# Kernel optimization log

Hardware: AMD Instinct MI355X
Metric: run time of the kernel (lower is better)

The kernel has to match this reference:

```python
import jax, jax.numpy as jnp
import numpy as np

DIM = 64  # per-head feature dim used for the 1/sqrt(dim) scale


def setup_inputs() -> dict:
    key = jax.random.key(0)
    kq, kk, kv, kw, kb = jax.random.split(key, 5)
    B, S, D, DK = 32, 4096, 64, 256
    q = jax.random.normal(kq, (B, S, D), dtype=jnp.float32)
    k = jax.random.normal(kk, (B, S, D), dtype=jnp.float32)
    v = jax.random.normal(kv, (B, S, D), dtype=jnp.float32)
    # Linear(input_size=S -> dim_k=DK): weight [DK, S], bias [DK]
    E_w = jax.random.normal(kw, (DK, S), dtype=jnp.float32) * (1.0 / np.sqrt(S))
    E_b = jax.random.normal(kb, (DK,), dtype=jnp.float32) * 0.01
    return {"q": q, "k": k, "v": v, "E_w": E_w, "E_b": E_b}


def reference(q, k, v, E_w, E_b):
    # K projection: k.transpose(1,2) -> [b, d, s]; E(k) -> [b, d, dim_k]
    K = jnp.einsum('bsd,ks->bdk', k, E_w) + E_b  # [b, d, dim_k]
    # scores = q @ K / sqrt(dim) -> [b, s, dim_k]
    scores = jnp.matmul(q, K) / jnp.sqrt(jnp.asarray(DIM, q.dtype))
    P_bar = jax.nn.softmax(scores, axis=-1)  # softmax over projected dim_k axis
    # V projection with F = E (parameter sharing): v -> [b, d, dim_k] -> transpose -> [b, dim_k, d]
    V = jnp.einsum('bsd,ks->bkd', v, E_w) + E_b[None, :, None]  # [b, dim_k, d]
    out = jnp.matmul(P_bar, V)  # [b, s, d]
    return out
```

## Files before the change

### kernel.cpp

```cpp
#include <hip/hip_runtime.h>
#include <hip/hip_bf16.h>
#include <stdint.h>

#define B_  32
#define S_  4096
#define D_  64
#define DK_ 256

typedef float f32x4 __attribute__((ext_vector_type(4)));
typedef short s16x8 __attribute__((ext_vector_type(8)));
typedef uint32_t u32x4 __attribute__((ext_vector_type(4)));

static __device__ __forceinline__ uint16_t f2bf(float f) {
    union { float f; uint32_t u; } x; x.f = f;
    uint32_t u = x.u;
    u += 0x7FFFu + ((u >> 16) & 1u);
    return (uint16_t)(u >> 16);
}

static __device__ __forceinline__ float bf2f(uint32_t hi16) {
    union { uint32_t u; float f; } x; x.u = hi16;
    return x.f;
}

static __device__ __forceinline__ uint32_t pk2(float a, float b) {
    __hip_bfloat162 h = __float22bfloat162_rn(float2{a, b});
    union { __hip_bfloat162 h; uint32_t u; } c; c.h = h;
    return c.u;
}

static __device__ __forceinline__ void gload_lds16(const uint16_t* g, uint16_t* l) {
    __builtin_amdgcn_global_load_lds(
        (const __attribute__((address_space(1))) uint32_t*)g,
        (__attribute__((address_space(3))) uint32_t*)l, 16, 0, 0);
}

__global__ __launch_bounds__(256) void ewcvt(const float* __restrict__ E_w,
                                             uint16_t* __restrict__ EwbS) {
    const int tg     = blockIdx.x * 256 + threadIdx.x;
    const int l16    = tg & 15;
    const int grp    = (tg >> 4) & 3;
    const int schunk = (tg >> 6) & 127;
    const int kktile = tg >> 13;
    const int kk = kktile*16 + l16;
    const int s  = schunk*32 + grp*8;
    const float4 f0 = *(const float4*)(E_w + (size_t)kk * S_ + s);
    const float4 f1 = *(const float4*)(E_w + (size_t)kk * S_ + s + 4);
    s16x8 o;
    o[0] = (short)f2bf(f0.x); o[1] = (short)f2bf(f0.y);
    o[2] = (short)f2bf(f0.z); o[3] = (short)f2bf(f0.w);
    o[4] = (short)f2bf(f1.x); o[5] = (short)f2bf(f1.y);
    o[6] = (short)f2bf(f1.z); o[7] = (short)f2bf(f1.w);
    *(s16x8*)(EwbS + (size_t)tg * 8) = o;
}

__global__ __launch_bounds__(256, 4) void proj_mfma(
        const uint16_t* __restrict__ EwbS,
        const float* __restrict__ kin, const float* __restrict__ vin,
        uint32_t* __restrict__ part) {
    const int bid = blockIdx.x;
    const int ss = bid & 15;
    const int b  = (bid >> 4) & 31;
    const int p  = bid >> 9;
    const float* x = (p ? vin : kin) + (size_t)b * S_ * D_;
    uint32_t* outp = part + ((size_t)((p*32 + b)*16 + ss)) * 8192;

    __shared__ __align__(16) uint16_t Bx[32 * 512];

    const int tid  = threadIdx.x;
    const int w    = tid >> 6;
    const int lane = tid & 63;
    const int l16  = lane & 15;
    const int grp  = lane >> 4;

    {
        const int dcol = tid & 63;
        const float* srcB = x + ((size_t)(ss*256 + w*8)) * D_ + dcol;
        const int boff0 = ((dcol >> 4) << 9) + ((w*16 + (dcol & 15)) << 3);
        #pragma unroll
        for (int ks = 0; ks < 8; ++ks) {
            const float* sB = srcB + (size_t)ks*32*D_;
            float xv[8];
            #pragma unroll
            for (int i = 0; i < 8; ++i) xv[i] = sB[i * D_];
            s16x8 h;
            #pragma unroll
            for (int i = 0; i < 8; ++i) h[i] = (short)f2bf(xv[i]);
            *(s16x8*)&Bx[(ks << 11) + boff0] = h;
        }
    }
    __syncthreads();

    const uint16_t* aBase = EwbS + ((size_t)(w*4)*128 + ss*8) * 512 + lane*8;
    f32x4 acc[4][4] = {};
    #pragma unroll
    for (int ks = 0; ks < 8; ++ks) {
        s16x8 bf[4];
        #pragma unroll
        for (int nt = 0; nt < 4; ++nt)
            bf[nt] = *(const s16x8*)&Bx[((ks*4 + nt) << 9) + lane*8];
        #pragma unroll
        for (int m = 0; m < 4; ++m) {
            const s16x8 af = *(const s16x8*)(aBase + ((size_t)m*128 + ks) * 512);
            #pragma unroll
            for (int nt = 0; nt < 4; ++nt)
                acc[m][nt] = __builtin_amdgcn_mfma_f32_16x16x32_bf16(af, bf[nt], acc[m][nt], 0, 0, 0);
        }
    }

    #pragma unroll
    for (int m = 0; m < 4; ++m) {
        const int kkrow = w*64 + m*16 + grp*4;
        #pragma unroll
        for (int nt = 0; nt < 4; ++nt) {
            const int didx = nt*16 + l16;
            outp[didx*128 + (kkrow >> 1)]     = pk2(acc[m][nt][0], acc[m][nt][1]);
            outp[didx*128 + (kkrow >> 1) + 1] = pk2(acc[m][nt][2], acc[m][nt][3]);
        }
    }
}

__global__ __launch_bounds__(256) void bias_reduce(
        const uint32_t* __restrict__ part, const float* __restrict__ E_b,
        uint16_t* __restrict__ Kbf, uint16_t* __restrict__ Vbf) {
    const int b  = blockIdx.x >> 3;
    const int dt = blockIdx.x & 7;
    const int t  = threadIdx.x;

    __shared__ uint16_t Kt[256][10];

    const uint32_t* Kp = part + ((size_t)(b*16))      * 8192 + dt*8*128;
    const uint32_t* Vp = part + ((size_t)((32+b)*16)) * 8192 + dt*8*128;

    #pragma unroll
    for (int j = 0; j < 4; ++j) {
        const int idx = j*256 + t;
        const int d_l = idx >> 7;
        const int kkp = idx & 127;
        float k0 = 0.f, k1 = 0.f, v0 = 0.f, v1 = 0.f;
        #pragma unroll
        for (int s = 0; s < 16; ++s) {
            const uint32_t ku = Kp[(size_t)s*8192 + d_l*128 + kkp];
            const uint32_t vu = Vp[(size_t)s*8192 + d_l*128 + kkp];
            k0 += bf2f(ku << 16);
            k1 += bf2f(ku & 0xffff0000u);
            v0 += bf2f(vu << 16);
            v1 += bf2f(vu & 0xffff0000u);
        }
        const int kk0 = kkp*2;
        const float b0 = E_b[kk0], b1 = E_b[kk0 + 1];
        *(uint32_t*)(Vbf + ((size_t)(b*64 + dt*8 + d_l))*256 + kk0) =
            (uint32_t)f2bf(v0 + b0) | ((uint32_t)f2bf(v1 + b1) << 16);
        Kt[kk0][d_l]     = f2bf(k0 + b0);
        Kt[kk0 + 1][d_l] = f2bf(k1 + b1);
    }
    __syncthreads();

    uint16_t* kout = Kbf + ((size_t)(b*256 + t))*64 + dt*8;
    s16x8 o0;
    #pragma unroll
    for (int i = 0; i < 8; ++i) o0[i] = (short)Kt[t][i];
    *(s16x8*)kout = o0;
}

__global__ __launch_bounds__(512, 4) void attn(
        const float* __restrict__ q,
        const uint16_t* __restrict__ Kbf, const uint16_t* __restrict__ Vbf,
        float* __restrict__ out) {
    const int wg   = blockIdx.x;
    const int st   = wg & 31;
    const int b    = wg >> 5;
    const int tid  = threadIdx.x;
    const int wave = tid >> 6;
    const int lane = tid & 63;
    const int l16  = lane & 15;
    const int grp  = lane >> 4;
    const int s0   = st * 128 + wave * 16;

    __shared__ __align__(16) uint16_t Klds[16384];
    __shared__ __align__(16) uint16_t Vlds[16384];

    const uint16_t* Kb = Kbf + (size_t)b * DK_ * D_;
    const uint16_t* Vb = Vbf + (size_t)b * D_ * DK_;

    #pragma unroll
    for (int i = 0; i < 4; ++i) {
        const int s  = wave*4 + i;
        const int nt = s >> 1, kt = s & 1;
        gload_lds16(Kb + (size_t)(nt*16 + l16) * D_ + kt*32 + grp*8, &Klds[s*512]);
    }
    #pragma unroll
    for (int i = 0; i < 4; ++i) {
        const int s   = wave*4 + i;
        const int kt2 = s >> 2, nt2 = s & 3;
        gload_lds16(Vb + (size_t)(nt2*16 + l16) * DK_ + kt2*32 + grp*8, &Vlds[s*512]);
    }

    s16x8 qb[2];
    {
        const float* qp = q + ((size_t)b * S_ + s0 + l16) * D_;
        #pragma unroll
        for (int kt = 0; kt < 2; ++kt) {
            const int d0 = kt*32 + grp*8;
            const float4 f0 = *(const float4*)(qp + d0);
            const float4 f1 = *(const float4*)(qp + d0 + 4);
            s16x8 a;
            a[0] = (short)f2bf(f0.x * 0.125f);
            a[1] = (short)f2bf(f0.y * 0.125f);
            a[2] = (short)f2bf(f0.z * 0.125f);
            a[3] = (short)f2bf(f0.w * 0.125f);
            a[4] = (short)f2bf(f1.x * 0.125f);
            a[5] = (short)f2bf(f1.y * 0.125f);
            a[6] = (short)f2bf(f1.z * 0.125f);
            a[7] = (short)f2bf(f1.w * 0.125f);
            qb[kt] = a;
        }
    }

    __syncthreads();

    f32x4 acc[16] = {};
    #pragma unroll
    for (int nt = 0; nt < 16; ++nt) {
        #pragma unroll
        for (int kt = 0; kt < 2; ++kt) {
            const s16x8 kf = *(const s16x8*)&Klds[(nt*2 + kt)*512 + lane*8];
            acc[nt] = __builtin_amdgcn_mfma_f32_16x16x32_bf16(kf, qb[kt], acc[nt], 0, 0, 0);
        }
    }

    float sm = 0.f;
    #pragma unroll
    for (int nt = 0; nt < 16; ++nt) {
        #pragma unroll
        for (int r = 0; r < 4; ++r) {
            const float e = __expf(acc[nt][r]);
            acc[nt][r] = e;
            sm += e;
        }
    }
    sm += __shfl_xor(sm, 16);
    sm += __shfl_xor(sm, 32);
    const float inv = 1.f / sm;

    uint32_t pk[16][2];
    #pragma unroll
    for (int nt = 0; nt < 16; ++nt) {
        pk[nt][0] = pk2(acc[nt][0], acc[nt][1]);
        pk[nt][1] = pk2(acc[nt][2], acc[nt][3]);
    }

    float invs[4];
    #pragma unroll
    for (int r = 0; r < 4; ++r) invs[r] = __shfl(inv, grp*4 + r);

    const int sl0 = (((grp << 1) + 0) & 3) * 16 + l16;
    const int sl1 = (((grp << 1) + 1) & 3) * 16 + l16;
    const bool lohalf = (grp < 2);

    f32x4 o[4] = {};
    #pragma unroll
    for (int kt2 = 0; kt2 < 8; ++kt2) {
        union { u32x4 wv; s16x8 h; } u;
        #pragma unroll
        for (int c = 0; c < 4; ++c) {
            const int tt = c & 1;
            const int sl = (c >> 1) ? sl1 : sl0;
            const uint32_t lo = (uint32_t)__shfl((int)pk[2*kt2 + 0][tt], sl);
            const uint32_t hi = (uint32_t)__shfl((int)pk[2*kt2 + 1][tt], sl);
            u.wv[c] = lohalf ? lo : hi;
        }
        #pragma unroll
        for (int nt2 = 0; nt2 < 4; ++nt2) {
            const s16x8 vf = *(const s16x8*)&Vlds[(kt2*4 + nt2)*512 + lane*8];
            o[nt2] = __builtin_amdgcn_mfma_f32_16x16x32_bf16(u.h, vf, o[nt2], 0, 0, 0);
        }
    }

    #pragma unroll
    for (int nt2 = 0; nt2 < 4; ++nt2)
        #pragma unroll
        for (int r = 0; r < 4; ++r)
            out[((size_t)b * S_ + s0 + grp*4 + r) * D_ + nt2*16 + l16] =
                o[nt2][r] * invs[r];
}

extern "C" void kernel_launch(void* const* d_in, const int* in_sizes, int n_in,
                              void* d_out, int out_size, void* d_ws, size_t ws_size,
                              hipStream_t stream) {
    const float* q   = (const float*)d_in[0];
    const float* k   = (const float*)d_in[1];
    const float* v   = (const float*)d_in[2];
    const float* E_w = (const float*)d_in[3];
    const float* E_b = (const float*)d_in[4];
    float* out = (float*)d_out;

    char* ws = (char*)d_ws;
    uint32_t* part = (uint32_t*)(ws);
    uint16_t* Kbf  = (uint16_t*)(ws + (32u << 20));
    uint16_t* Vbf  = (uint16_t*)(ws + (33u << 20));
    uint16_t* EwbS = (uint16_t*)(ws + (34u << 20));

    ewcvt<<<512, 256, 0, stream>>>(E_w, EwbS);
    proj_mfma<<<1024, 256, 0, stream>>>(EwbS, k, v, part);
    bias_reduce<<<256, 256, 0, stream>>>(part, E_b, Kbf, Vbf);
    attn<<<1024, 512, 0, stream>>>(q, Kbf, Vbf, out);
}
```

Baseline: 67.13 us.

## Give each projection block four S-chunks with double-buffered LDS and fewer partials

Each proj_mfma block now covers 1024 sequence rows instead of 256. It loops over four sub-chunks and prefetches the next chunk's k/v into registers while the MFMAs run on the current LDS buffer. This cuts the partial-sum buffer and the bias_reduce reduction from 16 partials to 4, which lowers global write/read traffic and the grid size. The trade-offs are fewer blocks (256 on a large GPU), heavy register use (64 prefetch floats) and double the LDS, which may reduce occupancy and latency hiding.

```diff
diff --git a/kernel.cpp b/kernel.cpp
--- a/kernel.cpp
+++ b/kernel.cpp
@@ -54,18 +54,18 @@
     *(s16x8*)(EwbS + (size_t)tg * 8) = o;
 }
 
-__global__ __launch_bounds__(256, 4) void proj_mfma(
+__global__ __launch_bounds__(256) void proj_mfma(
         const uint16_t* __restrict__ EwbS,
         const float* __restrict__ kin, const float* __restrict__ vin,
         uint32_t* __restrict__ part) {
     const int bid = blockIdx.x;
-    const int ss = bid & 15;
-    const int b  = (bid >> 4) & 31;
-    const int p  = bid >> 9;
+    const int ss = bid & 3;
+    const int b  = (bid >> 2) & 31;
+    const int p  = bid >> 7;
     const float* x = (p ? vin : kin) + (size_t)b * S_ * D_;
-    uint32_t* outp = part + ((size_t)((p*32 + b)*16 + ss)) * 8192;
-
-    __shared__ __align__(16) uint16_t Bx[32 * 512];
+    uint32_t* outp = part + ((size_t)((p*32 + b)*4 + ss)) * 8192;
+
+    __shared__ __align__(16) uint16_t Bx[2][32 * 512];
 
     const int tid  = threadIdx.x;
     const int w    = tid >> 6;
@@ -73,39 +73,65 @@
     const int l16  = lane & 15;
     const int grp  = lane >> 4;
 
-    {
-        const int dcol = tid & 63;
-        const float* srcB = x + ((size_t)(ss*256 + w*8)) * D_ + dcol;
-        const int boff0 = ((dcol >> 4) << 9) + ((w*16 + (dcol & 15)) << 3);
+    const int dcol = tid & 63;
+    const float* srcB = x + ((size_t)(ss*1024 + w*8)) * D_ + dcol;
+    const int boff0 = ((dcol >> 4) << 9) + ((w*16 + (dcol & 15)) << 3);
+
+    #pragma unroll
+    for (int ks = 0; ks < 8; ++ks) {
+        const float* sB = srcB + (size_t)ks*32*D_;
+        float xv[8];
+        #pragma unroll
+        for (int i = 0; i < 8; ++i) xv[i] = sB[i * D_];
+        s16x8 h;
+        #pragma unroll
+        for (int i = 0; i < 8; ++i) h[i] = (short)f2bf(xv[i]);
+        *(s16x8*)&Bx[0][(ks << 11) + boff0] = h;
+    }
+    __syncthreads();
+
+    const uint16_t* aBase = EwbS + ((size_t)(w*4)*128 + ss*32) * 512 + lane*8;
+    f32x4 acc[4][4] = {};
+
+    #pragma unroll
+    for (int sup = 0; sup < 4; ++sup) {
+        float xv[64];
+        if (sup < 3) {
+            const float* sS = srcB + (size_t)(sup+1)*256*D_;
+            #pragma unroll
+            for (int ks = 0; ks < 8; ++ks)
+                #pragma unroll
+                for (int i = 0; i < 8; ++i)
+                    xv[ks*8 + i] = sS[(size_t)(ks*32 + i) * D_];
+        }
+
+        const uint16_t* bufc = &Bx[sup & 1][0];
         #pragma unroll
         for (int ks = 0; ks < 8; ++ks) {
-            const float* sB = srcB + (size_t)ks*32*D_;
-            float xv[8];
-            #pragma unroll
-            for (int i = 0; i < 8; ++i) xv[i] = sB[i * D_];
-            s16x8 h;
-            #pragma unroll
-            for (int i = 0; i < 8; ++i) h[i] = (short)f2bf(xv[i]);
-            *(s16x8*)&Bx[(ks << 11) + boff0] = h;
-        }
-    }
-    __syncthreads();
-
-    const uint16_t* aBase = EwbS + ((size_t)(w*4)*128 + ss*8) * 512 + lane*8;
-    f32x4 acc[4][4] = {};
-    #pragma unroll
-    for (int ks = 0; ks < 8; ++ks) {
-        s16x8 bf[4];
-        #pragma unroll
-        for (int nt = 0; nt < 4; ++nt)
-            bf[nt] = *(const s16x8*)&Bx[((ks*4 + nt) << 9) + lane*8];
-        #pragma unroll
-        for (int m = 0; m < 4; ++m) {
-            const s16x8 af = *(const s16x8*)(aBase + ((size_t)m*128 + ks) * 512);
+            s16x8 bf[4];
             #pragma unroll
             for (int nt = 0; nt < 4; ++nt)
-                acc[m][nt] = __builtin_amdgcn_mfma_f32_16x16x32_bf16(af, bf[nt], acc[m][nt], 0, 0, 0);
-        }
+                bf[nt] = *(const s16x8*)&bufc[((ks*4 + nt) << 9) + lane*8];
+            #pragma unroll
+            for (int m = 0; m < 4; ++m) {
+                const s16x8 af = *(const s16x8*)(aBase + ((size_t)m*128 + sup*8 + ks) * 512);
+                #pragma unroll
+                for (int nt = 0; nt < 4; ++nt)
+                    acc[m][nt] = __builtin_amdgcn_mfma_f32_16x16x32_bf16(af, bf[nt], acc[m][nt], 0, 0, 0);
+            }
+        }
+
+        if (sup < 3) {
+            uint16_t* bufn = &Bx[(sup + 1) & 1][0];
+            #pragma unroll
+            for (int ks = 0; ks < 8; ++ks) {
+                s16x8 h;
+                #pragma unroll
+                for (int i = 0; i < 8; ++i) h[i] = (short)f2bf(xv[ks*8 + i]);
+                *(s16x8*)&bufn[(ks << 11) + boff0] = h;
+            }
+        }
+        __syncthreads();
     }
 
     #pragma unroll
@@ -129,8 +155,8 @@
 
     __shared__ uint16_t Kt[256][10];
 
-    const uint32_t* Kp = part + ((size_t)(b*16))      * 8192 + dt*8*128;
-    const uint32_t* Vp = part + ((size_t)((32+b)*16)) * 8192 + dt*8*128;
+    const uint32_t* Kp = part + ((size_t)(b*4))      * 8192 + dt*8*128;
+    const uint32_t* Vp = part + ((size_t)((32+b)*4)) * 8192 + dt*8*128;
 
     #pragma unroll
     for (int j = 0; j < 4; ++j) {
@@ -139,7 +165,7 @@
         const int kkp = idx & 127;
         float k0 = 0.f, k1 = 0.f, v0 = 0.f, v1 = 0.f;
         #pragma unroll
-        for (int s = 0; s < 16; ++s) {
+        for (int s = 0; s < 4; ++s) {
             const uint32_t ku = Kp[(size_t)s*8192 + d_l*128 + kkp];
             const uint32_t vu = Vp[(size_t)s*8192 + d_l*128 + kkp];
             k0 += bf2f(ku << 16);
@@ -297,12 +323,12 @@
 
     char* ws = (char*)d_ws;
     uint32_t* part = (uint32_t*)(ws);
-    uint16_t* Kbf  = (uint16_t*)(ws + (32u << 20));
-    uint16_t* Vbf  = (uint16_t*)(ws + (33u << 20));
-    uint16_t* EwbS = (uint16_t*)(ws + (34u << 20));
+    uint16_t* Kbf  = (uint16_t*)(ws + (8u  << 20));
+    uint16_t* Vbf  = (uint16_t*)(ws + (9u  << 20));
+    uint16_t* EwbS = (uint16_t*)(ws + (10u << 20));
 
     ewcvt<<<512, 256, 0, stream>>>(E_w, EwbS);
-    proj_mfma<<<1024, 256, 0, stream>>>(EwbS, k, v, part);
+    proj_mfma<<<256, 256, 0, stream>>>(EwbS, k, v, part);
     bias_reduce<<<256, 256, 0, stream>>>(part, E_b, Kbf, Vbf);
     attn<<<1024, 512, 0, stream>>>(q, Kbf, Vbf, out);
 }
```

After: 65.54 us. 1.02x faster.
